# Performance work log

Measured on AMD Instinct MI355X. Metric: run time of the kernel, lower is better.

## Reference

```python
import jax, jax.numpy as jnp
import numpy as np

N_NODES = 50000
N_EDGES = 400000
F_IN = 128
HID = 64
HEADS = 8
N_CLASSES = 16
NEG_SLOPE = 0.2  # PyG GATConv default negative_slope


def _glorot(key, shape):
    fan_in, fan_out = shape[0], shape[-1]
    lim = jnp.sqrt(6.0 / (fan_in + fan_out))
    return jax.random.uniform(key, shape, jnp.float32, -lim, lim)


def setup_inputs() -> dict:
    key = jax.random.key(0)
    ks = jax.random.split(key, 16)
    x = jax.random.normal(ks[0], (N_NODES, F_IN), jnp.float32)
    edge_index = jax.random.randint(ks[1], (2, N_EDGES), 0, N_NODES, jnp.int64)
    # layer 0: F_IN -> HEADS*HID (concat)
    W0 = _glorot(ks[2], (F_IN, HEADS * HID))
    a_s0 = _glorot(ks[3], (HEADS, HID))
    a_d0 = _glorot(ks[4], (HEADS, HID))
    b0 = jnp.zeros((HEADS * HID,), jnp.float32)
    # layer 1: HEADS*HID -> HEADS*HID (concat)
    W1 = _glorot(ks[5], (HEADS * HID, HEADS * HID))
    a_s1 = _glorot(ks[6], (HEADS, HID))
    a_d1 = _glorot(ks[7], (HEADS, HID))
    b1 = jnp.zeros((HEADS * HID,), jnp.float32)
    # final layer: HEADS*HID -> N_CLASSES, heads=1, concat=False (mean over heads)
    W2 = _glorot(ks[8], (HEADS * HID, 1 * N_CLASSES))
    a_s2 = _glorot(ks[9], (1, N_CLASSES))
    a_d2 = _glorot(ks[10], (1, N_CLASSES))
    b2 = jnp.zeros((N_CLASSES,), jnp.float32)
    return {"x": x, "edge_index": edge_index,
            "W0": W0, "a_s0": a_s0, "a_d0": a_d0, "b0": b0,
            "W1": W1, "a_s1": a_s1, "a_d1": a_d1, "b1": b1,
            "W2": W2, "a_s2": a_s2, "a_d2": a_d2, "b2": b2}


def gat_conv(x, src, dst, W, a_src, a_dst, b, num_nodes, concat):
    """One PyG-style GATConv (self-loops already in src/dst).
    x: [N, F_in]; W: [F_in, H*C]; a_src/a_dst: [H, C]; b: [H*C] or [C]."""
    H, C = a_src.shape
    h = (x @ W).reshape(num_nodes, H, C)                    # [N,H,C]
    al_s = jnp.einsum('nhc,hc->nh', h, a_src)               # [N,H]
    al_d = jnp.einsum('nhc,hc->nh', h, a_dst)               # [N,H]
    e = jax.nn.leaky_relu(al_s[src] + al_d[dst], NEG_SLOPE) # [E,H]
    # scatter-softmax over incoming edges of each destination node
    m = jax.ops.segment_max(e, dst, num_segments=num_nodes)  # [N,H]
    ex = jnp.exp(e - m[dst])
    denom = jax.ops.segment_sum(ex, dst, num_segments=num_nodes)
    alpha = ex / denom[dst]                                  # [E,H]
    out = jax.ops.segment_sum(alpha[:, :, None] * h[src], dst,
                              num_segments=num_nodes)        # [N,H,C]
    if concat:
        return out.reshape(num_nodes, H * C) + b
    return out.mean(axis=1) + b


def reference(x, edge_index, W0, a_s0, a_d0, b0, W1, a_s1, a_d1, b1,
              W2, a_s2, a_d2, b2):
    N = x.shape[0]
    # PyG GATConv adds self-loops by default
    loops = jnp.arange(N, dtype=edge_index.dtype)
    src = jnp.concatenate([edge_index[0], loops])
    dst = jnp.concatenate([edge_index[1], loops])
    h = gat_conv(x, src, dst, W0, a_s0, a_d0, b0, N, concat=True)
    h = jax.nn.elu(h)  # dropout is identity in eval mode
    h = gat_conv(h, src, dst, W1, a_s1, a_d1, b1, N, concat=True)
    h = jax.nn.elu(h)
    return gat_conv(h, src, dst, W2, a_s2, a_d2, b2, N, concat=False)
```

## Files before the change

kernel.cpp:

```cpp
#include <hip/hip_runtime.h>

#define N_NODES 50000
#define N_EDGES 400000
#define E_TOT   450000
#define NEG 0.2f
#define NB_SCAN ((N_NODES + 255) / 256)

typedef unsigned short ushort_t;
typedef __attribute__((ext_vector_type(8))) short  short8;
typedef __attribute__((ext_vector_type(4))) float  f32x4;
typedef __attribute__((ext_vector_type(8))) unsigned short ushort8;

__device__ __forceinline__ ushort_t f2bf(float f){
    union { float f; unsigned u; } v; v.f = f;
    unsigned u = v.u;
    return (ushort_t)((u + 0x7FFFu + ((u >> 16) & 1u)) >> 16);
}
__device__ __forceinline__ float bflo(unsigned u){
    union { unsigned u; float f; } v; v.u = u << 16; return v.f;
}
__device__ __forceinline__ float bfhi(unsigned u){
    union { unsigned u; float f; } v; v.u = u & 0xFFFF0000u; return v.f;
}
__device__ __forceinline__ void gload_lds16(const void* g, void* l){
    __builtin_amdgcn_global_load_lds((const __attribute__((address_space(1))) void*)g,
                                     (__attribute__((address_space(3))) void*)l, 16, 0, 0);
}
__device__ __forceinline__ int wave_incl_scan(int v, int lane){
    #pragma unroll
    for(int off = 1; off < 64; off <<= 1){
        int t = __shfl_up(v, off, 64);
        if(lane >= off) v += t;
    }
    return v;
}


__global__ void zero_ints(int* p, int n){
    int i = blockIdx.x*256 + threadIdx.x;
    if(i < n) p[i] = 0;
}

__global__ void count_deg(const int* __restrict__ ei, int* __restrict__ deg){
    int e = blockIdx.x*256 + threadIdx.x;
    if(e >= E_TOT) return;
    int dst = (e < N_EDGES) ? ei[N_EDGES + e] : (e - N_EDGES);
    atomicAdd(&deg[dst], 1);
}

__global__ void deg_block_sum(const int* __restrict__ deg, int* __restrict__ bsum){
    int i = blockIdx.x*256 + threadIdx.x;
    int lane = threadIdx.x & 63, wave = threadIdx.x >> 6;
    int v = (i < N_NODES) ? deg[i] : 0;
    #pragma unroll
    for(int off = 1; off < 64; off <<= 1) v += __shfl_xor(v, off, 64);
    __shared__ int sw[4];
    if(lane == 0) sw[wave] = v;
    __syncthreads();
    if(threadIdx.x == 0) bsum[blockIdx.x] = sw[0] + sw[1] + sw[2] + sw[3];
}

__global__ void scan_bsum(int* __restrict__ bsum, int* __restrict__ rowptr){
    int lane = threadIdx.x & 63, wave = threadIdx.x >> 6;
    int v = (threadIdx.x < NB_SCAN) ? bsum[threadIdx.x] : 0;
    int incl = wave_incl_scan(v, lane);
    __shared__ int sw[4];
    if(lane == 63) sw[wave] = incl;
    __syncthreads();
    int add = 0;
    for(int w = 0; w < wave; w++) add += sw[w];
    int excl = incl - v + add;
    if(threadIdx.x < NB_SCAN) bsum[threadIdx.x] = excl;
    if(threadIdx.x == 255) rowptr[N_NODES] = excl + v;
}

__global__ void scan_apply(const int* __restrict__ bsum,
                           int* __restrict__ dw, int* __restrict__ rowptr){
    int i = blockIdx.x*256 + threadIdx.x;
    int lane = threadIdx.x & 63, wave = threadIdx.x >> 6;
    int v = (i < N_NODES) ? dw[i] : 0;
    int incl = wave_incl_scan(v, lane);
    __shared__ int sw[4];
    if(lane == 63) sw[wave] = incl;
    __syncthreads();
    int add = bsum[blockIdx.x];
    for(int w = 0; w < wave; w++) add += sw[w];
    int excl = incl - v + add;
    if(i < N_NODES){ rowptr[i] = excl; dw[i] = excl; }
}

__global__ void scatter_edges(const int* __restrict__ ei, int* __restrict__ wofs,
                              int* __restrict__ csr){
    int e = blockIdx.x*256 + threadIdx.x;
    if(e >= E_TOT) return;
    int src, dst;
    if(e < N_EDGES){ src = ei[e]; dst = ei[N_EDGES + e]; }
    else { src = dst = e - N_EDGES; }
    int pos = atomicAdd(&wofs[dst], 1);
    csr[pos] = src;
}


__global__ void cvt_all(const float* __restrict__ x, const float* __restrict__ W0,
                        const float* __restrict__ W1,
                        ushort_t* __restrict__ xbf, ushort_t* __restrict__ W0t,
                        ushort_t* __restrict__ W1t){
    int i = blockIdx.x*256 + threadIdx.x;
    if(i < N_NODES*128) xbf[i] = f2bf(x[i]);
    if(i < 512*128){ int n = i >> 7, k = i & 127; W0t[i] = f2bf(W0[(size_t)k*512 + n]); }
    if(i < 512*512){ int n = i >> 9, k = i & 511; W1t[i] = f2bf(W1[(size_t)k*512 + n]); }
}


template<int K>
__global__ __launch_bounds__(256) void gemm_bt(const ushort_t* __restrict__ A,
                                               const ushort_t* __restrict__ Bt,
                                               ushort_t* __restrict__ Cb,
                                               const float* __restrict__ a_s,
                                               const float* __restrict__ a_d,
                                               float* __restrict__ als,
                                               float* __restrict__ ald, int M){
    __shared__ ushort_t As[128*32];
    __shared__ ushort_t Bs[128*32];
    int tid  = threadIdx.x;
    int wave = tid >> 6, lane = tid & 63;
    int wm = wave & 1, wn = wave >> 1;
    int row0 = blockIdx.y * 128;
    int col0 = blockIdx.x * 128;

    f32x4 acc[4][4] = {};

    int lrow = lane >> 2;
    int lchk = (lane & 3) * 8;

    for(int kt = 0; kt < K; kt += 32){
        #pragma unroll
        for(int s = 0; s < 2; s++){
            int seg = wave*2 + s;
            int ar = row0 + seg*16 + lrow;
            ar = ar < M ? ar : M-1;
            gload_lds16(A  + (size_t)ar*K + kt + lchk, As + seg*512);
            int br = col0 + seg*16 + lrow;
            gload_lds16(Bt + (size_t)br*K + kt + lchk, Bs + seg*512);
        }
        __syncthreads();

        short8 a[4], b[4];
        int fm = lane & 15, fq = (lane >> 4) * 8;
        #pragma unroll
        for(int t = 0; t < 4; t++){
            a[t] = *(const short8*)&As[(wm*64 + t*16 + fm)*32 + fq];
            b[t] = *(const short8*)&Bs[(wn*64 + t*16 + fm)*32 + fq];
        }
        #pragma unroll
        for(int i = 0; i < 4; i++)
            #pragma unroll
            for(int j = 0; j < 4; j++)
                acc[i][j] = __builtin_amdgcn_mfma_f32_16x16x32_bf16(a[i], b[j], acc[i][j], 0, 0, 0);
        __syncthreads();
    }

    int cm = (lane >> 4) * 4, cn = lane & 15;
    int head = (col0 + wn*64) >> 6;
    float as_[4], ad_[4];
    #pragma unroll
    for(int j = 0; j < 4; j++){
        int c = head*64 + cn + j*16;
        as_[j] = a_s[c]; ad_[j] = a_d[c];
    }
    #pragma unroll
    for(int i = 0; i < 4; i++){
        #pragma unroll
        for(int p = 0; p < 4; p++){
            int r = row0 + wm*64 + i*16 + cm + p;
            float ps = 0.f, pd = 0.f;
            if(r < M){
                ushort_t* cp = &Cb[(size_t)r*512 + col0 + wn*64 + cn];
                #pragma unroll
                for(int j = 0; j < 4; j++){
                    float v = acc[i][j][p];
                    cp[j*16] = f2bf(v);
                    ps += v*as_[j]; pd += v*ad_[j];
                }
            }
            #pragma unroll
            for(int off = 1; off < 16; off <<= 1){
                ps += __shfl_xor(ps, off);
                pd += __shfl_xor(pd, off);
            }
            if(cn == 0 && r < M){ als[r*8 + head] = ps; ald[r*8 + head] = pd; }
        }
    }
}


__global__ __launch_bounds__(256) void attn_agg(const ushort_t* __restrict__ h,
        const float* __restrict__ als, const float* __restrict__ ald,
        const int* __restrict__ rowptr, const int* __restrict__ csr,
        const float* __restrict__ bias, ushort_t* __restrict__ out){
    __shared__ float sm[4][8], sd[4][8];
    int wv = threadIdx.x >> 6, lane = threadIdx.x & 63;
    int n = blockIdx.x*4 + wv;
    int start = rowptr[n], end = rowptr[n+1];

    int hd = lane & 7, e8 = lane >> 3;
    float aldv = ald[n*8 + hd];
    float lmax = -1e30f;
    for(int idx = start + e8; idx < end; idx += 8){
        int src = csr[idx];
        float v = als[src*8 + hd] + aldv;
        v = v > 0.f ? v : NEG*v;
        lmax = fmaxf(lmax, v);
    }
    for(int off = 8; off < 64; off <<= 1) lmax = fmaxf(lmax, __shfl_xor(lmax, off));
    float lsum = 0.f;
    for(int idx = start + e8; idx < end; idx += 8){
        int src = csr[idx];
        float v = als[src*8 + hd] + aldv;
        v = v > 0.f ? v : NEG*v;
        lsum += __expf(v - lmax);
    }
    for(int off = 8; off < 64; off <<= 1) lsum += __shfl_xor(lsum, off);
    if(lane < 8){ sm[wv][hd] = lmax; sd[wv][hd] = 1.f / lsum; }
    __syncthreads();

    int head = lane >> 3;
    float m = sm[wv][head], inv = sd[wv][head];
    float aldn = ald[n*8 + head];
    float acc[8] = {};

    int last = end - 1;
    for(int idx = start; idx < end; idx += 4){
        int j1 = idx+1, j2 = idx+2, j3 = idx+3;
        int s0 = csr[idx];
        int s1 = csr[j1 <= last ? j1 : last];
        int s2 = csr[j2 <= last ? j2 : last];
        int s3 = csr[j3 <= last ? j3 : last];
        uint4 p0 = *(const uint4*)&h[(size_t)s0*512 + lane*8];
        uint4 p1 = *(const uint4*)&h[(size_t)s1*512 + lane*8];
        uint4 p2 = *(const uint4*)&h[(size_t)s2*512 + lane*8];
        uint4 p3 = *(const uint4*)&h[(size_t)s3*512 + lane*8];
        float v0 = als[s0*8 + head] + aldn; v0 = v0 > 0.f ? v0 : NEG*v0;
        float v1 = als[s1*8 + head] + aldn; v1 = v1 > 0.f ? v1 : NEG*v1;
        float v2 = als[s2*8 + head] + aldn; v2 = v2 > 0.f ? v2 : NEG*v2;
        float v3 = als[s3*8 + head] + aldn; v3 = v3 > 0.f ? v3 : NEG*v3;
        float e0 = __expf(v0 - m);
        float e1 = (j1 < end) ? __expf(v1 - m) : 0.f;
        float e2 = (j2 < end) ? __expf(v2 - m) : 0.f;
        float e3 = (j3 < end) ? __expf(v3 - m) : 0.f;
        acc[0] += e0*bflo(p0.x) + e1*bflo(p1.x) + e2*bflo(p2.x) + e3*bflo(p3.x);
        acc[1] += e0*bfhi(p0.x) + e1*bfhi(p1.x) + e2*bfhi(p2.x) + e3*bfhi(p3.x);
        acc[2] += e0*bflo(p0.y) + e1*bflo(p1.y) + e2*bflo(p2.y) + e3*bflo(p3.y);
        acc[3] += e0*bfhi(p0.y) + e1*bfhi(p1.y) + e2*bfhi(p2.y) + e3*bfhi(p3.y);
        acc[4] += e0*bflo(p0.z) + e1*bflo(p1.z) + e2*bflo(p2.z) + e3*bflo(p3.z);
        acc[5] += e0*bfhi(p0.z) + e1*bfhi(p1.z) + e2*bfhi(p2.z) + e3*bfhi(p3.z);
        acc[6] += e0*bflo(p0.w) + e1*bflo(p1.w) + e2*bflo(p2.w) + e3*bflo(p3.w);
        acc[7] += e0*bfhi(p0.w) + e1*bfhi(p1.w) + e2*bfhi(p2.w) + e3*bfhi(p3.w);
    }

    ushort8 o;
    #pragma unroll
    for(int j = 0; j < 8; j++){
        float v = acc[j]*inv + bias[lane*8 + j];
        v = v > 0.f ? v : (__expf(v) - 1.f);
        o[j] = f2bf(v);
    }
    *(ushort8*)&out[(size_t)n*512 + lane*8] = o;
}


__global__ __launch_bounds__(256) void gemm2_k(const ushort_t* __restrict__ A,
                                               const float* __restrict__ W,
                                               const float* __restrict__ a_s2,
                                               const float* __restrict__ a_d2,
                                               float* __restrict__ C,
                                               float* __restrict__ als,
                                               float* __restrict__ ald){
    __shared__ float Ws[16][513];
    for(int i = threadIdx.x; i < 512*16; i += 256){
        int k = i >> 4, c = i & 15;
        Ws[c][k] = W[i];
    }
    __syncthreads();
    int t = blockIdx.x*256 + threadIdx.x;
    int c = t & 15;
    long row = t >> 4;
    const ushort_t* ap = &A[row*512];
    const float* wp = &Ws[c][0];
    float acc = 0.f;
    for(int k = 0; k < 512; k += 8){
        uint4 p = *(const uint4*)&ap[k];
        acc += bflo(p.x)*wp[k+0] + bfhi(p.x)*wp[k+1]
             + bflo(p.y)*wp[k+2] + bfhi(p.y)*wp[k+3]
             + bflo(p.z)*wp[k+4] + bfhi(p.z)*wp[k+5]
             + bflo(p.w)*wp[k+6] + bfhi(p.w)*wp[k+7];
    }
    C[t] = acc;
    float ps = acc * a_s2[c], pd = acc * a_d2[c];
    #pragma unroll
    for(int off = 1; off < 16; off <<= 1){
        ps += __shfl_xor(ps, off);
        pd += __shfl_xor(pd, off);
    }
    if(c == 0){ als[row] = ps; ald[row] = pd; }
}

__global__ __launch_bounds__(256) void attn_agg2(const float* __restrict__ h2,
        const float* __restrict__ als, const float* __restrict__ ald,
        const int* __restrict__ rowptr, const int* __restrict__ csr,
        const float* __restrict__ b2, float* __restrict__ out){
    int wv = threadIdx.x >> 6, lane = threadIdx.x & 63;
    int q = lane >> 4, c = lane & 15;
    int n = blockIdx.x*16 + wv*4 + q;
    int start = rowptr[n], end = rowptr[n+1];
    float aldv = ald[n];

    float lmax = -1e30f;
    for(int idx = start + c; idx < end; idx += 16){
        float v = als[csr[idx]] + aldv; v = v > 0.f ? v : NEG*v;
        lmax = fmaxf(lmax, v);
    }
    #pragma unroll
    for(int off = 1; off < 16; off <<= 1) lmax = fmaxf(lmax, __shfl_xor(lmax, off));
    float lsum = 0.f;
    for(int idx = start + c; idx < end; idx += 16){
        float v = als[csr[idx]] + aldv; v = v > 0.f ? v : NEG*v;
        lsum += __expf(v - lmax);
    }
    #pragma unroll
    for(int off = 1; off < 16; off <<= 1) lsum += __shfl_xor(lsum, off);
    float inv = 1.f / lsum;

    float acc = 0.f;
    for(int idx = start; idx < end; idx++){
        int src = csr[idx];
        float v = als[src] + aldv; v = v > 0.f ? v : NEG*v;
        float alpha = __expf(v - lmax) * inv;
        acc += alpha * h2[src*16 + c];
    }
    out[n*16 + c] = acc + b2[c];
}


extern "C" void kernel_launch(void* const* d_in, const int* in_sizes, int n_in,
                              void* d_out, int out_size, void* d_ws, size_t ws_size,
                              hipStream_t stream) {
    const float* x    = (const float*)d_in[0];
    const int*   ei   = (const int*)  d_in[1];
    const float* W0   = (const float*)d_in[2];
    const float* a_s0 = (const float*)d_in[3];
    const float* a_d0 = (const float*)d_in[4];
    const float* b0   = (const float*)d_in[5];
    const float* W1   = (const float*)d_in[6];
    const float* a_s1 = (const float*)d_in[7];
    const float* a_d1 = (const float*)d_in[8];
    const float* b1   = (const float*)d_in[9];
    const float* W2   = (const float*)d_in[10];
    const float* a_s2 = (const float*)d_in[11];
    const float* a_d2 = (const float*)d_in[12];
    const float* b2   = (const float*)d_in[13];
    float* out = (float*)d_out;

    char* w = (char*)d_ws;
    auto alloc = [&](size_t bytes){ void* p = (void*)w; w += (bytes + 255) & ~(size_t)255; return p; };
    int*      rowptr = (int*)     alloc((N_NODES+1)*sizeof(int));
    int*      wofs   = (int*)     alloc(N_NODES*sizeof(int));
    int*      bsum   = (int*)     alloc(NB_SCAN*sizeof(int));
    int*      csr    = (int*)     alloc(E_TOT*sizeof(int));
    float*    als    = (float*)   alloc((size_t)N_NODES*8*sizeof(float));
    float*    ald    = (float*)   alloc((size_t)N_NODES*8*sizeof(float));
    ushort_t* hb     = (ushort_t*)alloc((size_t)N_NODES*512*sizeof(ushort_t));
    ushort_t* hbf    = (ushort_t*)alloc((size_t)N_NODES*512*sizeof(ushort_t));
    ushort_t* xbf    = (ushort_t*)alloc((size_t)N_NODES*128*sizeof(ushort_t));
    ushort_t* W0t    = (ushort_t*)alloc((size_t)512*128*sizeof(ushort_t));
    ushort_t* W1t    = (ushort_t*)alloc((size_t)512*512*sizeof(ushort_t));
    float*    h2     = (float*)   alloc((size_t)N_NODES*16*sizeof(float));

    zero_ints<<<(N_NODES+255)/256, 256, 0, stream>>>(wofs, N_NODES);
    count_deg<<<(E_TOT+255)/256, 256, 0, stream>>>(ei, wofs);
    deg_block_sum<<<NB_SCAN, 256, 0, stream>>>(wofs, bsum);
    scan_bsum<<<1, 256, 0, stream>>>(bsum, rowptr);
    scan_apply<<<NB_SCAN, 256, 0, stream>>>(bsum, wofs, rowptr);
    scatter_edges<<<(E_TOT+255)/256, 256, 0, stream>>>(ei, wofs, csr);

    cvt_all<<<(N_NODES*128+255)/256, 256, 0, stream>>>(x, W0, W1, xbf, W0t, W1t);

    gemm_bt<128><<<dim3(4, (N_NODES+127)/128), 256, 0, stream>>>(xbf, W0t, hb, a_s0, a_d0, als, ald, N_NODES);
    attn_agg<<<N_NODES/4, 256, 0, stream>>>(hb, als, ald, rowptr, csr, b0, hbf);

    gemm_bt<512><<<dim3(4, (N_NODES+127)/128), 256, 0, stream>>>(hbf, W1t, hb, a_s1, a_d1, als, ald, N_NODES);
    attn_agg<<<N_NODES/4, 256, 0, stream>>>(hb, als, ald, rowptr, csr, b1, hbf);

    gemm2_k<<<(N_NODES*16)/256, 256, 0, stream>>>(hbf, W2, a_s2, a_d2, h2, als, ald);
    attn_agg2<<<N_NODES/16, 256, 0, stream>>>(h2, als, ald, rowptr, csr, b2, out);
}
```

Measured before the change: 462.0 us.

## Switch intermediates to fp16 and cache attention exponents in LDS

Replaces the bf16 storage and MFMA with fp16 (f16 MFMA, half conversions) across the GEMMs, the aggregation and the final projection. In attn_agg, the leaky-relu logits and then their exponentials are kept in shared memory for the first 64 edges per node. This avoids recomputing the gathers and exps in the second and third passes, and edges beyond that limit fall back to the recompute path. The cost is extra LDS per block (4*64*8 floats) and fp16 range and overflow risk on the activations.

```diff
diff --git a/kernel.cpp b/kernel.cpp
--- a/kernel.cpp
+++ b/kernel.cpp
@@ -5,22 +5,22 @@
 #define E_TOT   450000
 #define NEG 0.2f
 #define NB_SCAN ((N_NODES + 255) / 256)
+#define MAXD 64
 
 typedef unsigned short ushort_t;
-typedef __attribute__((ext_vector_type(8))) short  short8;
+typedef __attribute__((ext_vector_type(8))) _Float16 half8;
 typedef __attribute__((ext_vector_type(4))) float  f32x4;
 typedef __attribute__((ext_vector_type(8))) unsigned short ushort8;
 
-__device__ __forceinline__ ushort_t f2bf(float f){
-    union { float f; unsigned u; } v; v.f = f;
-    unsigned u = v.u;
-    return (ushort_t)((u + 0x7FFFu + ((u >> 16) & 1u)) >> 16);
-}
-__device__ __forceinline__ float bflo(unsigned u){
-    union { unsigned u; float f; } v; v.u = u << 16; return v.f;
-}
-__device__ __forceinline__ float bfhi(unsigned u){
-    union { unsigned u; float f; } v; v.u = u & 0xFFFF0000u; return v.f;
+__device__ __forceinline__ ushort_t f2h(float f){
+    _Float16 h = (_Float16)f;
+    union { _Float16 h; ushort_t u; } v; v.h = h; return v.u;
+}
+__device__ __forceinline__ float h_lo(unsigned u){
+    union { unsigned u; _Float16 h[2]; } v; v.u = u; return (float)v.h[0];
+}
+__device__ __forceinline__ float h_hi(unsigned u){
+    union { unsigned u; _Float16 h[2]; } v; v.u = u; return (float)v.h[1];
 }
 __device__ __forceinline__ void gload_lds16(const void* g, void* l){
     __builtin_amdgcn_global_load_lds((const __attribute__((address_space(1))) void*)g,
@@ -106,9 +106,9 @@
                         ushort_t* __restrict__ xbf, ushort_t* __restrict__ W0t,
                         ushort_t* __restrict__ W1t){
     int i = blockIdx.x*256 + threadIdx.x;
-    if(i < N_NODES*128) xbf[i] = f2bf(x[i]);
-    if(i < 512*128){ int n = i >> 7, k = i & 127; W0t[i] = f2bf(W0[(size_t)k*512 + n]); }
-    if(i < 512*512){ int n = i >> 9, k = i & 511; W1t[i] = f2bf(W1[(size_t)k*512 + n]); }
+    if(i < N_NODES*128) xbf[i] = f2h(x[i]);
+    if(i < 512*128){ int n = i >> 7, k = i & 127; W0t[i] = f2h(W0[(size_t)k*512 + n]); }
+    if(i < 512*512){ int n = i >> 9, k = i & 511; W1t[i] = f2h(W1[(size_t)k*512 + n]); }
 }
 
 
@@ -145,18 +145,18 @@
         }
         __syncthreads();
 
-        short8 a[4], b[4];
+        half8 a[4], b[4];
         int fm = lane & 15, fq = (lane >> 4) * 8;
         #pragma unroll
         for(int t = 0; t < 4; t++){
-            a[t] = *(const short8*)&As[(wm*64 + t*16 + fm)*32 + fq];
-            b[t] = *(const short8*)&Bs[(wn*64 + t*16 + fm)*32 + fq];
+            a[t] = *(const half8*)&As[(wm*64 + t*16 + fm)*32 + fq];
+            b[t] = *(const half8*)&Bs[(wn*64 + t*16 + fm)*32 + fq];
         }
         #pragma unroll
         for(int i = 0; i < 4; i++)
             #pragma unroll
             for(int j = 0; j < 4; j++)
-                acc[i][j] = __builtin_amdgcn_mfma_f32_16x16x32_bf16(a[i], b[j], acc[i][j], 0, 0, 0);
+                acc[i][j] = __builtin_amdgcn_mfma_f32_16x16x32_f16(a[i], b[j], acc[i][j], 0, 0, 0);
         __syncthreads();
     }
 
@@ -179,7 +179,7 @@
                 #pragma unroll
                 for(int j = 0; j < 4; j++){
                     float v = acc[i][j][p];
-                    cp[j*16] = f2bf(v);
+                    cp[j*16] = f2h(v);
                     ps += v*as_[j]; pd += v*ad_[j];
                 }
             }
@@ -199,6 +199,7 @@
         const int* __restrict__ rowptr, const int* __restrict__ csr,
         const float* __restrict__ bias, ushort_t* __restrict__ out){
     __shared__ float sm[4][8], sd[4][8];
+    __shared__ float sex[4][MAXD][8];
     int wv = threadIdx.x >> 6, lane = threadIdx.x & 63;
     int n = blockIdx.x*4 + wv;
     int start = rowptr[n], end = rowptr[n+1];
@@ -207,30 +208,37 @@
     float aldv = ald[n*8 + hd];
     float lmax = -1e30f;
     for(int idx = start + e8; idx < end; idx += 8){
+        int e = idx - start;
         int src = csr[idx];
         float v = als[src*8 + hd] + aldv;
         v = v > 0.f ? v : NEG*v;
+        if(e < MAXD) sex[wv][e][hd] = v;
         lmax = fmaxf(lmax, v);
     }
     for(int off = 8; off < 64; off <<= 1) lmax = fmaxf(lmax, __shfl_xor(lmax, off));
     float lsum = 0.f;
     for(int idx = start + e8; idx < end; idx += 8){
-        int src = csr[idx];
-        float v = als[src*8 + hd] + aldv;
-        v = v > 0.f ? v : NEG*v;
-        lsum += __expf(v - lmax);
+        int e = idx - start;
+        float v;
+        if(e < MAXD) v = sex[wv][e][hd];
+        else { int src = csr[idx]; v = als[src*8 + hd] + aldv; v = v > 0.f ? v : NEG*v; }
+        float ex = __expf(v - lmax);
+        if(e < MAXD) sex[wv][e][hd] = ex;
+        lsum += ex;
     }
     for(int off = 8; off < 64; off <<= 1) lsum += __shfl_xor(lsum, off);
     if(lane < 8){ sm[wv][hd] = lmax; sd[wv][hd] = 1.f / lsum; }
     __syncthreads();
 
     int head = lane >> 3;
-    float m = sm[wv][head], inv = sd[wv][head];
-    float aldn = ald[n*8 + head];
+    float inv = sd[wv][head];
     float acc[8] = {};
 
-    int last = end - 1;
-    for(int idx = start; idx < end; idx += 4){
+    int cnt = end - start;
+    int nmain = cnt < MAXD ? cnt : MAXD;
+    int mend = start + nmain;
+    int last = mend - 1;
+    for(int idx = start; idx < mend; idx += 4){
         int j1 = idx+1, j2 = idx+2, j3 = idx+3;
         int s0 = csr[idx];
         int s1 = csr[j1 <= last ? j1 : last];
@@ -240,22 +248,33 @@
         uint4 p1 = *(const uint4*)&h[(size_t)s1*512 + lane*8];
         uint4 p2 = *(const uint4*)&h[(size_t)s2*512 + lane*8];
         uint4 p3 = *(const uint4*)&h[(size_t)s3*512 + lane*8];
-        float v0 = als[s0*8 + head] + aldn; v0 = v0 > 0.f ? v0 : NEG*v0;
-        float v1 = als[s1*8 + head] + aldn; v1 = v1 > 0.f ? v1 : NEG*v1;
-        float v2 = als[s2*8 + head] + aldn; v2 = v2 > 0.f ? v2 : NEG*v2;
-        float v3 = als[s3*8 + head] + aldn; v3 = v3 > 0.f ? v3 : NEG*v3;
-        float e0 = __expf(v0 - m);
-        float e1 = (j1 < end) ? __expf(v1 - m) : 0.f;
-        float e2 = (j2 < end) ? __expf(v2 - m) : 0.f;
-        float e3 = (j3 < end) ? __expf(v3 - m) : 0.f;
-        acc[0] += e0*bflo(p0.x) + e1*bflo(p1.x) + e2*bflo(p2.x) + e3*bflo(p3.x);
-        acc[1] += e0*bfhi(p0.x) + e1*bfhi(p1.x) + e2*bfhi(p2.x) + e3*bfhi(p3.x);
-        acc[2] += e0*bflo(p0.y) + e1*bflo(p1.y) + e2*bflo(p2.y) + e3*bflo(p3.y);
-        acc[3] += e0*bfhi(p0.y) + e1*bfhi(p1.y) + e2*bfhi(p2.y) + e3*bfhi(p3.y);
-        acc[4] += e0*bflo(p0.z) + e1*bflo(p1.z) + e2*bflo(p2.z) + e3*bflo(p3.z);
-        acc[5] += e0*bfhi(p0.z) + e1*bfhi(p1.z) + e2*bfhi(p2.z) + e3*bfhi(p3.z);
-        acc[6] += e0*bflo(p0.w) + e1*bflo(p1.w) + e2*bflo(p2.w) + e3*bflo(p3.w);
-        acc[7] += e0*bfhi(p0.w) + e1*bfhi(p1.w) + e2*bfhi(p2.w) + e3*bfhi(p3.w);
+        float e0 = sex[wv][idx -start][head];
+        float e1 = (j1 < mend) ? sex[wv][j1-start][head] : 0.f;
+        float e2 = (j2 < mend) ? sex[wv][j2-start][head] : 0.f;
+        float e3 = (j3 < mend) ? sex[wv][j3-start][head] : 0.f;
+        acc[0] += e0*h_lo(p0.x) + e1*h_lo(p1.x) + e2*h_lo(p2.x) + e3*h_lo(p3.x);
+        acc[1] += e0*h_hi(p0.x) + e1*h_hi(p1.x) + e2*h_hi(p2.x) + e3*h_hi(p3.x);
+        acc[2] += e0*h_lo(p0.y) + e1*h_lo(p1.y) + e2*h_lo(p2.y) + e3*h_lo(p3.y);
+        acc[3] += e0*h_hi(p0.y) + e1*h_hi(p1.y) + e2*h_hi(p2.y) + e3*h_hi(p3.y);
+        acc[4] += e0*h_lo(p0.z) + e1*h_lo(p1.z) + e2*h_lo(p2.z) + e3*h_lo(p3.z);
+        acc[5] += e0*h_hi(p0.z) + e1*h_hi(p1.z) + e2*h_hi(p2.z) + e3*h_hi(p3.z);
+        acc[6] += e0*h_lo(p0.w) + e1*h_lo(p1.w) + e2*h_lo(p2.w) + e3*h_lo(p3.w);
+        acc[7] += e0*h_hi(p0.w) + e1*h_hi(p1.w) + e2*h_hi(p2.w) + e3*h_hi(p3.w);
+    }
+    if(mend < end){
+        float m = sm[wv][head];
+        float aldn = ald[n*8 + head];
+        for(int idx = mend; idx < end; idx++){
+            int src = csr[idx];
+            float v = als[src*8 + head] + aldn;
+            v = v > 0.f ? v : NEG*v;
+            float e0 = __expf(v - m);
+            uint4 p = *(const uint4*)&h[(size_t)src*512 + lane*8];
+            acc[0] += e0*h_lo(p.x); acc[1] += e0*h_hi(p.x);
+            acc[2] += e0*h_lo(p.y); acc[3] += e0*h_hi(p.y);
+            acc[4] += e0*h_lo(p.z); acc[5] += e0*h_hi(p.z);
+            acc[6] += e0*h_lo(p.w); acc[7] += e0*h_hi(p.w);
+        }
     }
 
     ushort8 o;
@@ -263,7 +282,7 @@
     for(int j = 0; j < 8; j++){
         float v = acc[j]*inv + bias[lane*8 + j];
         v = v > 0.f ? v : (__expf(v) - 1.f);
-        o[j] = f2bf(v);
+        o[j] = f2h(v);
     }
     *(ushort8*)&out[(size_t)n*512 + lane*8] = o;
 }
@@ -290,10 +309,10 @@
     float acc = 0.f;
     for(int k = 0; k < 512; k += 8){
         uint4 p = *(const uint4*)&ap[k];
-        acc += bflo(p.x)*wp[k+0] + bfhi(p.x)*wp[k+1]
-             + bflo(p.y)*wp[k+2] + bfhi(p.y)*wp[k+3]
-             + bflo(p.z)*wp[k+4] + bfhi(p.z)*wp[k+5]
-             + bflo(p.w)*wp[k+6] + bfhi(p.w)*wp[k+7];
+        acc += h_lo(p.x)*wp[k+0] + h_hi(p.x)*wp[k+1]
+             + h_lo(p.y)*wp[k+2] + h_hi(p.y)*wp[k+3]
+             + h_lo(p.z)*wp[k+4] + h_hi(p.z)*wp[k+5]
+             + h_lo(p.w)*wp[k+6] + h_hi(p.w)*wp[k+7];
     }
     C[t] = acc;
     float ps = acc * a_s2[c], pd = acc * a_d2[c];
```

After: 463.9 us. No clear change (+0.4%).
